# Kernel tuning notes

Measured on AMD Instinct MI355X. Metric: run time of the kernel, lower is better.

The kernel has to match this reference:

```python
import jax, jax.numpy as jnp
import numpy as np

B, IN, H, F, T = 4096, 1024, 1024, 128, 3
LN_EPS = 1e-5


def setup_inputs() -> dict:
    key = jax.random.key(0)
    ks = jax.random.split(key, 12)
    inp = {
        "input_": jax.random.normal(ks[0], (B, IN), jnp.float32),
        "hx": jax.random.normal(ks[1], (B, H), jnp.float32),
        "cx": jax.random.normal(ks[2], (B, H), jnp.float32),
        "topic_w": jax.random.uniform(ks[3], (B, T), jnp.float32),
        # factorized gate weights (init scales per reset_parameters)
        "w_ih_a": jax.random.normal(ks[4], (4 * H, F), jnp.float32) / jnp.sqrt(F),
        "w_ih_b": jnp.full((F, T), 0.1 / T, jnp.float32),
        "w_ih_c": jax.random.normal(ks[5], (F, IN), jnp.float32) / jnp.sqrt(IN),
        "w_hh_a": 0.1 * jax.random.normal(ks[6], (4 * H, F), jnp.float32),
        "w_hh_b": jnp.full((F, T), 0.1 / T, jnp.float32),
        "w_hh_c": 0.1 * jax.random.normal(ks[7], (F, H), jnp.float32),
        # theta transforms: weight=0, bias=1 per reset_parameters
        "th_ih_w": jnp.zeros((T, T), jnp.float32),
        "th_ih_b": jnp.ones((T,), jnp.float32),
        "th_hh_w": jnp.zeros((T, T), jnp.float32),
        "th_hh_b": jnp.ones((T,), jnp.float32),
        # layernorm params
        "ln_i_w": jnp.ones((4 * H,), jnp.float32),
        "ln_i_b": jnp.zeros((4 * H,), jnp.float32),
        "ln_h_w": jnp.ones((4 * H,), jnp.float32),
        "ln_h_b": jnp.zeros((4 * H,), jnp.float32),
        "ln_c_w": jnp.ones((H,), jnp.float32),
        "ln_c_b": jnp.zeros((H,), jnp.float32),
    }
    return inp


def _ln(x, w, b):
    mu = x.mean(-1, keepdims=True)
    var = ((x - mu) ** 2).mean(-1, keepdims=True)
    return (x - mu) * jax.lax.rsqrt(var + LN_EPS) * w + b


def reference(input_, hx, cx, topic_w,
              w_ih_a, w_ih_b, w_ih_c, w_hh_a, w_hh_b, w_hh_c,
              th_ih_w, th_ih_b, th_hh_w, th_hh_b,
              ln_i_w, ln_i_b, ln_h_w, ln_h_b, ln_c_w, ln_c_b):
    # factorized input gates: ((x @ C^T) * (theta(topic) @ B^T)) @ A^T
    scale_i = (topic_w @ th_ih_w.T + th_ih_b) @ w_ih_b.T            # [B, F]
    igates = ((input_ @ w_ih_c.T) * scale_i) @ w_ih_a.T             # [B, 4H]
    scale_h = (topic_w @ th_hh_w.T + th_hh_b) @ w_hh_b.T            # [B, F]
    hgates = ((hx @ w_hh_c.T) * scale_h) @ w_hh_a.T                 # [B, 4H]

    gates = _ln(igates, ln_i_w, ln_i_b) + _ln(hgates, ln_h_w, ln_h_b)
    i, f, g, o = jnp.split(gates, 4, axis=1)
    i = jax.nn.sigmoid(i)
    f = jax.nn.sigmoid(f)
    g = jnp.tanh(g)  # dropout p=0 -> identity
    o = jax.nn.sigmoid(o)
    cy = _ln(f * cx + i * g, ln_c_w, ln_c_b)
    hy = o * jnp.tanh(cy)
    return hy, cy
```

## Files before the change

### kernel.cpp

```cpp
#include <hip/hip_runtime.h>

typedef unsigned short ushort_t;
typedef __attribute__((ext_vector_type(8))) short bf8_t;
typedef __attribute__((ext_vector_type(4))) float f4_t;

#define B_   4096
#define IN_  1024
#define H_   1024
#define F_   128
#define EPS_ 1e-5f

#define NG1   512
#define NPREP 256
#define NGRAM 128

#define KC_   64
#define NCH_  16
#define XSZ_  4096
#define WSZ_  32768
#define LDSZ_ 36864

__device__ __forceinline__ float us2f(unsigned short s) {
  union { unsigned int u; float f; } v;
  v.u = ((unsigned int)s) << 16;
  return v.f;
}
__device__ __forceinline__ unsigned short f2us(float f) {
  union { float f; unsigned int u; } v;
  v.f = f;
  unsigned int r = (v.u + 0x7fffu + ((v.u >> 16) & 1u)) >> 16;
  return (unsigned short)r;
}
__device__ __forceinline__ float sigf(float x) { return 1.0f / (1.0f + __expf(-x)); }
__device__ __forceinline__ float tanh_f(float x) { return 1.0f - 2.0f / (1.0f + __expf(2.0f * x)); }

__device__ __forceinline__ int detect_fp32(const void* disc) {
  return ((const unsigned int*)disc)[0] == 0x3F800000u;
}
__device__ __forceinline__ float ldf(const void* p, int i, int fp32) {
  return fp32 ? ((const float*)p)[i] : us2f(((const ushort_t*)p)[i]);
}
__device__ __forceinline__ void ld8(const void* p, int idx, float* o, int fp32) {
  if (fp32) {
    const float4* q = (const float4*)((const float*)p + idx);
    float4 v0 = q[0], v1 = q[1];
    o[0]=v0.x; o[1]=v0.y; o[2]=v0.z; o[3]=v0.w;
    o[4]=v1.x; o[5]=v1.y; o[6]=v1.z; o[7]=v1.w;
  } else {
    uint4 v = *(const uint4*)((const ushort_t*)p + idx);
    const ushort_t* pv = (const ushort_t*)&v;
    #pragma unroll
    for (int i = 0; i < 8; i++) o[i] = us2f(pv[i]);
  }
}
__device__ __forceinline__ bf8_t cvt8p(const float* f) {
  union { bf8_t v; unsigned int u[4]; } r;
  const unsigned int* ui = (const unsigned int*)f;
  #pragma unroll
  for (int i = 0; i < 4; i++) {
    unsigned int lo = ui[2 * i] + 0x8000u;
    unsigned int hi = ui[2 * i + 1] + 0x8000u;
    r.u[i] = __builtin_amdgcn_perm(hi, lo, 0x07060302u);
  }
  return r.v;
}

__device__ __forceinline__ void gl_lds16(const void* g, void* l) {
  __builtin_amdgcn_global_load_lds(
      (const __attribute__((address_space(1))) unsigned int*)g,
      (__attribute__((address_space(3))) unsigned int*)l, 16, 0, 0);
}

__global__ __launch_bounds__(256, 4) void k_stageA(
    const void* __restrict__ X0, const void* __restrict__ X1,
    const void* __restrict__ Wc0, const void* __restrict__ Wc1,
    const void* __restrict__ Ai, const void* __restrict__ Ah,
    const void* __restrict__ lnwi, const void* __restrict__ lnwh,
    ushort_t* __restrict__ wb,
    float* __restrict__ cm_i, float* __restrict__ cm_h,
    float* __restrict__ g_i, float* __restrict__ g_h,
    float* __restrict__ C0, float* __restrict__ C1)
{
  __shared__ __align__(16) char lds_raw[LDSZ_];
  int bid = blockIdx.x, tid = threadIdx.x;
  int fp32 = detect_fp32(lnwi);

  if (bid < NG1) {
    int rb = bid >> 1, mat = bid & 1;
    const char* Xc = (const char*)(mat ? X1 : X0);
    const char* Wc = (const char*)(mat ? Wc1 : Wc0);
    float* C = mat ? C1 : C0;
    int lane = tid & 63, w = tid >> 6;
    int quad = lane >> 4, lcol = lane & 15;
    int brow0 = rb * 16;

    const char* srcp[9];
    #pragma unroll
    for (int j = 0; j < 9; j++) {
      int flat = (w * 9 + j) * 1024 + (lane << 4);
      if (flat < XSZ_) {
        int r = flat >> 8, inb = flat & 255;
        srcp[j] = Xc + (size_t)(brow0 + r) * 4096 + (inb ^ ((r & 7) << 5));
      } else {
        int fw = flat - XSZ_;
        int r = fw >> 8, inb = fw & 255;
        srcp[j] = Wc + (size_t)r * 4096 + (inb ^ ((r & 7) << 5));
      }
    }

    f4_t acc[2];
    acc[0] = (f4_t){0.f, 0.f, 0.f, 0.f};
    acc[1] = (f4_t){0.f, 0.f, 0.f, 0.f};

    for (int kc0 = 0; kc0 < NCH_; kc0++) {
      int koff = kc0 * 256;
      #pragma unroll
      for (int j = 0; j < 9; j++)
        gl_lds16(srcp[j] + koff, lds_raw + (w * 9 + j) * 1024);
      __syncthreads();

      #pragma unroll
      for (int kc = 0; kc < 2; kc++) {
        int kb = kc * 128 + quad * 32;
        int abyte = lcol * 256 + (kb ^ ((lcol & 7) << 5));
        float4 a0 = *(const float4*)(lds_raw + abyte);
        float4 a1 = *(const float4*)(lds_raw + abyte + 16);
        float a8[8] = {a0.x, a0.y, a0.z, a0.w, a1.x, a1.y, a1.z, a1.w};
        bf8_t af = cvt8p(a8);
        #pragma unroll
        for (int t = 0; t < 2; t++) {
          int f = w * 32 + t * 16 + lcol;
          int wbyte = XSZ_ + f * 256 + (kb ^ ((f & 7) << 5));
          float4 b0 = *(const float4*)(lds_raw + wbyte);
          float4 b1 = *(const float4*)(lds_raw + wbyte + 16);
          float b8[8] = {b0.x, b0.y, b0.z, b0.w, b1.x, b1.y, b1.z, b1.w};
          acc[t] = __builtin_amdgcn_mfma_f32_16x16x32_bf16(af, cvt8p(b8), acc[t], 0, 0, 0);
        }
      }
      __syncthreads();
    }

    #pragma unroll
    for (int t = 0; t < 2; t++) {
      int f = w * 32 + t * 16 + lcol;
      #pragma unroll
      for (int reg = 0; reg < 4; reg++)
        C[(brow0 + quad * 4 + reg) * F_ + f] = acc[t][reg];
    }
  } else if (bid < NG1 + NPREP) {
    int t = bid - NG1;
    #pragma unroll
    for (int i = 0; i < 16; i++) {
      int e = i * 256 + tid;
      int c = e >> 9, l = (e >> 3) & 63, j = e & 7;
      int k = c * 32 + ((l >> 4) << 3) + j;
      int n = t * 16 + (l & 15);
      float v;
      if (k < 128) v = ldf(Ai, n * F_ + k, fp32) * ldf(lnwi, n, fp32);
      else         v = ldf(Ah, n * F_ + (k - 128), fp32) * ldf(lnwh, n, fp32);
      wb[(size_t)t * 4096 + e] = f2us(v);
    }
    const void* A = (tid < 128) ? Ai : Ah;
    float* cm = (tid < 128) ? cm_i : cm_h;
    int f = tid & 127;
    float s = 0.f;
    #pragma unroll
    for (int i = 0; i < 16; i++) s += ldf(A, (t * 16 + i) * F_ + f, fp32);
    atomicAdd(&cm[f], s);
  } else {
    int g = bid - (NG1 + NPREP);
    int fblk = g & 3, mat = (g >> 2) & 1, z = g >> 3;
    const void* A = mat ? Ah : Ai;
    float* G = mat ? g_h : g_i;
    float (*As)[128] = (float(*)[128])lds_raw;
    int f1_0 = fblk * 32;
    int tf2 = tid & 31, tf1 = tid >> 5;
    float acc[4][4] = {};
    int nbase = z * 256;
    for (int n0 = nbase; n0 < nbase + 256; n0 += 32) {
      #pragma unroll
      for (int j = 0; j < 2; j++) {
        int idx = tid + 256 * j;
        int nn = idx >> 4, f8 = (idx & 15) * 8;
        float t[8];
        ld8(A, (n0 + nn) * F_ + f8, t, fp32);
        #pragma unroll
        for (int i = 0; i < 8; i++) As[nn][f8 + i] = t[i];
      }
      __syncthreads();
      #pragma unroll 4
      for (int nn = 0; nn < 32; nn++) {
        float4 a1 = *(const float4*)&As[nn][f1_0 + 4 * tf1];
        float4 a2 = *(const float4*)&As[nn][4 * tf2];
        const float* x1 = (const float*)&a1;
        const float* x2 = (const float*)&a2;
        #pragma unroll
        for (int i = 0; i < 4; i++)
          #pragma unroll
          for (int j = 0; j < 4; j++) acc[i][j] += x1[i] * x2[j];
      }
      __syncthreads();
    }
    #pragma unroll
    for (int i = 0; i < 4; i++)
      #pragma unroll
      for (int j = 0; j < 4; j++)
        atomicAdd(&G[(f1_0 + 4 * tf1 + i) * F_ + 4 * tf2 + j], acc[i][j]);
  }
}

__global__ __launch_bounds__(1024) void k_fused2(
    const float* __restrict__ C0g, const float* __restrict__ C1g,
    const float* __restrict__ g_i, const float* __restrict__ g_h,
    const float* __restrict__ cm_i, const float* __restrict__ cm_h,
    const void* __restrict__ topic,
    const void* __restrict__ thw0, const void* __restrict__ thw1,
    const void* __restrict__ thb0, const void* __restrict__ thb1,
    const void* __restrict__ wsb0, const void* __restrict__ wsb1,
    const ushort_t* __restrict__ wb,
    const void* __restrict__ lniw, const void* __restrict__ lnib,
    const void* __restrict__ lnhw, const void* __restrict__ lnhb,
    const void* __restrict__ lncw, const void* __restrict__ lncb,
    const void* __restrict__ cx, float* __restrict__ out)
{
  __shared__ float Cs[2][16][132];
  __shared__ __align__(16) ushort_t xs[4096];
  __shared__ float buf[16][1028];
  __shared__ float obuf[16][1028];
  __shared__ float p1part[2][4][16];
  __shared__ float p2s[2][16];
  __shared__ float rs2_s[2][16];
  __shared__ float mrs_s[2][16];
  __shared__ float wpart[16][16][2];
  __shared__ float mu_s[16], rs_s[16];

  int tid = threadIdx.x;
  int lane = tid & 63, w = tid >> 6;
  int quad = lane >> 4, lcol = lane & 15;
  int b0 = blockIdx.x * 16;
  int fp32 = detect_fp32(lniw);

  {
    int mat = tid >> 9, rem = tid & 511;
    int row = rem >> 5, f0 = (rem & 31) * 4;
    const float* C = mat ? C1g : C0g;
    const void* thw = mat ? thw1 : thw0;
    const void* thb = mat ? thb1 : thb0;
    const void* wbp = mat ? wsb1 : wsb0;
    float tp0 = ldf(topic, (b0 + row) * 3 + 0, fp32);
    float tp1 = ldf(topic, (b0 + row) * 3 + 1, fp32);
    float tp2 = ldf(topic, (b0 + row) * 3 + 2, fp32);
    float tv[3];
    #pragma unroll
    for (int t = 0; t < 3; t++)
      tv[t] = ldf(thb, t, fp32) + tp0 * ldf(thw, t * 3 + 0, fp32)
            + tp1 * ldf(thw, t * 3 + 1, fp32) + tp2 * ldf(thw, t * 3 + 2, fp32);
    float4 v = *(const float4*)&C[(size_t)(b0 + row) * F_ + f0];
    const float* vp = (const float*)&v;
    #pragma unroll
    for (int j = 0; j < 4; j++) {
      int f = f0 + j;
      float sc = tv[0] * ldf(wbp, f * 3 + 0, fp32)
               + tv[1] * ldf(wbp, f * 3 + 1, fp32)
               + tv[2] * ldf(wbp, f * 3 + 2, fp32);
      Cs[mat][row][f] = vp[j] * sc;
    }
  }
  __syncthreads();

  if (w < 8) {
    int w2 = w & 3, smat = w >> 2;
    const float* G  = smat ? g_h : g_i;
    const float* cm = smat ? cm_h : cm_i;
    bf8_t af[4];
    float p2p = 0.f;
    #pragma unroll
    for (int kc = 0; kc < 4; kc++) {
      int kb = kc * 32 + quad * 8;
      float a[8];
      #pragma unroll
      for (int j = 0; j < 8; j++) a[j] = Cs[smat][lcol][kb + j];
      af[kc] = cvt8p(a);
      if (w2 == 0) {
        #pragma unroll
        for (int j = 0; j < 8; j++) p2p += a[j] * cm[kb + j];
      }
    }
    float p1p[4] = {0.f, 0.f, 0.f, 0.f};
    #pragma unroll
    for (int t = 0; t < 2; t++) {
      int colf = (w2 * 2 + t) * 16 + lcol;
      f4_t acc = {0.f, 0.f, 0.f, 0.f};
      #pragma unroll
      for (int kc = 0; kc < 4; kc++) {
        const float4* qg = (const float4*)(G + colf * F_ + kc * 32 + quad * 8);
        float4 w0 = qg[0], w1 = qg[1];
        float bt[8] = {w0.x, w0.y, w0.z, w0.w, w1.x, w1.y, w1.z, w1.w};
        acc = __builtin_amdgcn_mfma_f32_16x16x32_bf16(af[kc], cvt8p(bt), acc, 0, 0, 0);
      }
      #pragma unroll
      for (int reg = 0; reg < 4; reg++)
        p1p[reg] += acc[reg] * Cs[smat][quad * 4 + reg][colf];
    }
    #pragma unroll
    for (int d = 1; d < 16; d <<= 1)
      #pragma unroll
      for (int reg = 0; reg < 4; reg++)
        p1p[reg] += __shfl_xor(p1p[reg], d, 64);
    if (lcol == 0) {
      #pragma unroll
      for (int reg = 0; reg < 4; reg++)
        p1part[smat][w2][quad * 4 + reg] = p1p[reg];
    }
    if (w2 == 0) {
      p2p += __shfl_xor(p2p, 16, 64);
      p2p += __shfl_xor(p2p, 32, 64);
      if (quad == 0) p2s[smat][lcol] = p2p;
    }
  }
  __syncthreads();
  if (tid < 32) {
    int m = tid >> 4, r = tid & 15;
    float p1 = p1part[m][0][r] + p1part[m][1][r] + p1part[m][2][r] + p1part[m][3][r];
    float E2 = p1 * (1.0f / 4096.0f);
    float mu = p2s[m][r] * (1.0f / 4096.0f);
    float rs = rsqrtf(E2 - mu * mu + EPS_);
    rs2_s[m][r] = rs;
    mrs_s[m][r] = mu * rs;
  }
  __syncthreads();

  if (tid < 512) {
    int m = tid >> 8, tt = tid & 255;
    int f = tt & 127, half = tt >> 7;
    int k = m * 128 + f;
    int c = k >> 5, lq = (k >> 3) & 3, j = k & 7;
    #pragma unroll
    for (int i = 0; i < 8; i++) {
      int r2 = half * 8 + i;
      int lfrag = r2 | (lq << 4);
      xs[c * 512 + lfrag * 8 + j] = f2us(Cs[m][r2][f] * rs2_s[m][r2]);
    }
  }
  __syncthreads();

  float mi[4], mh[4];
  #pragma unroll
  for (int reg = 0; reg < 4; reg++) {
    mi[reg] = mrs_s[0][quad * 4 + reg];
    mh[reg] = mrs_s[1][quad * 4 + reg];
  }

  float s1[4] = {0.f, 0.f, 0.f, 0.f}, s2[4] = {0.f, 0.f, 0.f, 0.f};

  #pragma unroll
  for (int q = 0; q < 4; q++) {
    int cg = w * 4 + q;
    int col = cg * 16 + lcol;
    float cxv[4];
    #pragma unroll
    for (int reg = 0; reg < 4; reg++)
      cxv[reg] = ldf(cx, (size_t)(b0 + quad * 4 + reg) * H_ + col, fp32);

    f4_t accg[4];
    #pragma unroll
    for (int g = 0; g < 4; g++) accg[g] = (f4_t){0.f, 0.f, 0.f, 0.f};
    #pragma unroll
    for (int c = 0; c < 8; c++) {
      bf8_t af = *(const bf8_t*)&xs[c * 512 + lane * 8];
      #pragma unroll
      for (int g = 0; g < 4; g++) {
        bf8_t bf = *(const bf8_t*)(wb + (size_t)(g * 64 + cg) * 4096 + c * 512 + lane * 8);
        accg[g] = __builtin_amdgcn_mfma_f32_16x16x32_bf16(af, bf, accg[g], 0, 0, 0);
      }
    }
    float liw0 = ldf(lniw, 0 * H_ + col, fp32), lib0 = ldf(lnib, 0 * H_ + col, fp32);
    float lhw0 = ldf(lnhw, 0 * H_ + col, fp32), lhb0 = ldf(lnhb, 0 * H_ + col, fp32);
    float liw1 = ldf(lniw, 1 * H_ + col, fp32), lib1 = ldf(lnib, 1 * H_ + col, fp32);
    float lhw1 = ldf(lnhw, 1 * H_ + col, fp32), lhb1 = ldf(lnhb, 1 * H_ + col, fp32);
    float liw2 = ldf(lniw, 2 * H_ + col, fp32), lib2 = ldf(lnib, 2 * H_ + col, fp32);
    float lhw2 = ldf(lnhw, 2 * H_ + col, fp32), lhb2 = ldf(lnhb, 2 * H_ + col, fp32);
    float liw3 = ldf(lniw, 3 * H_ + col, fp32), lib3 = ldf(lnib, 3 * H_ + col, fp32);
    float lhw3 = ldf(lnhw, 3 * H_ + col, fp32), lhb3 = ldf(lnhb, 3 * H_ + col, fp32);
    #pragma unroll
    for (int reg = 0; reg < 4; reg++) {
      int m = quad * 4 + reg;
      float gi = accg[0][reg] + lib0 + lhb0 - mi[reg] * liw0 - mh[reg] * lhw0;
      float gf = accg[1][reg] + lib1 + lhb1 - mi[reg] * liw1 - mh[reg] * lhw1;
      float gg = accg[2][reg] + lib2 + lhb2 - mi[reg] * liw2 - mh[reg] * lhw2;
      float go = accg[3][reg] + lib3 + lhb3 - mi[reg] * liw3 - mh[reg] * lhw3;
      float iv = sigf(gi), fv = sigf(gf), gv = tanh_f(gg), ov = sigf(go);
      float cval = fv * cxv[reg] + iv * gv;
      buf[m][col] = cval;
      obuf[m][col] = ov;
      s1[reg] += cval;
      s2[reg] += cval * cval;
    }
  }

  #pragma unroll
  for (int d = 1; d < 16; d <<= 1) {
    #pragma unroll
    for (int reg = 0; reg < 4; reg++) {
      s1[reg] += __shfl_xor(s1[reg], d, 64);
      s2[reg] += __shfl_xor(s2[reg], d, 64);
    }
  }
  if (lcol == 0) {
    #pragma unroll
    for (int reg = 0; reg < 4; reg++) {
      wpart[w][quad * 4 + reg][0] = s1[reg];
      wpart[w][quad * 4 + reg][1] = s2[reg];
    }
  }
  __syncthreads();
  if (tid < 16) {
    float t1 = 0.f, t2 = 0.f;
    #pragma unroll
    for (int ww = 0; ww < 16; ww++) { t1 += wpart[ww][tid][0]; t2 += wpart[ww][tid][1]; }
    float mu = t1 * (1.0f / 1024.0f);
    float var = t2 * (1.0f / 1024.0f) - mu * mu;
    mu_s[tid] = mu;
    rs_s[tid] = rsqrtf(var + EPS_);
  }
  __syncthreads();

  #pragma unroll
  for (int q = 0; q < 4; q++) {
    int col = (w * 4 + q) * 16 + lcol;
    float lw = ldf(lncw, col, fp32), lb = ldf(lncb, col, fp32);
    #pragma unroll
    for (int reg = 0; reg < 4; reg++) {
      int m = quad * 4 + reg;
      float cyv = (buf[m][col] - mu_s[m]) * rs_s[m] * lw + lb;
      out[(size_t)B_ * H_ + (size_t)(b0 + m) * H_ + col] = cyv;
      out[(size_t)(b0 + m) * H_ + col] = obuf[m][col] * tanh_f(cyv);
    }
  }
}

extern "C" void kernel_launch(void* const* d_in, const int* in_sizes, int n_in,
                              void* d_out, int out_size, void* d_ws, size_t ws_size,
                              hipStream_t stream) {
  const void* input_  = d_in[0];
  const void* hx      = d_in[1];
  const void* cx      = d_in[2];
  const void* topic   = d_in[3];
  const void* w_ih_a  = d_in[4];
  const void* w_ih_b  = d_in[5];
  const void* w_ih_c  = d_in[6];
  const void* w_hh_a  = d_in[7];
  const void* w_hh_b  = d_in[8];
  const void* w_hh_c  = d_in[9];
  const void* th_ih_w = d_in[10];
  const void* th_ih_b = d_in[11];
  const void* th_hh_w = d_in[12];
  const void* th_hh_b = d_in[13];
  const void* ln_i_w  = d_in[14];
  const void* ln_i_b  = d_in[15];
  const void* ln_h_w  = d_in[16];
  const void* ln_h_b  = d_in[17];
  const void* ln_c_w  = d_in[18];
  const void* ln_c_b  = d_in[19];

  float* w = (float*)d_ws;
  float* c1    = w;
  float* c2    = c1 + B_ * F_;
  float* g_i   = c2 + B_ * F_;
  float* g_h   = g_i + F_ * F_;
  float* cm_i  = g_h + F_ * F_;
  float* cm_h  = cm_i + F_;
  ushort_t* wbf = (ushort_t*)(cm_h + F_);

  hipMemsetAsync(g_i, 0, (size_t)(2 * F_ * F_ + 2 * F_) * sizeof(float), stream);

  k_stageA<<<dim3(NG1 + NPREP + NGRAM), dim3(256), 0, stream>>>(
      input_, hx, w_ih_c, w_hh_c,
      w_ih_a, w_hh_a, ln_i_w, ln_h_w,
      wbf, cm_i, cm_h, g_i, g_h, c1, c2);
  k_fused2<<<dim3(256), dim3(1024), 0, stream>>>(
      c1, c2, g_i, g_h, cm_i, cm_h,
      topic, th_ih_w, th_hh_w, th_ih_b, th_hh_b, w_ih_b, w_hh_b,
      wbf, ln_i_w, ln_i_b, ln_h_w, ln_h_b, ln_c_w, ln_c_b, cx, (float*)d_out);
}
```

Baseline: 199.7 us.

## Merge stage kernels into one cooperative kernel with grid sync

Replaces the two-kernel pipeline with a single cooperative launch of 256 blocks of 1024 threads. Within each block, waves are split by role: the first 8 do the skinny x@C^T GEMM with double-buffered direct-to-LDS loads and per-wave waits, the next 4 prepare the packed weights and column means, and the last 4 compute the Gram matrix straight from global memory. A grid sync then runs the old second-stage code. This removes one kernel launch and overlaps the prep work with the GEMM, at the cost of a grid-wide barrier, a large 1024-thread footprint and a smaller union-shared LDS region for phase one.

Result: slower. 326.0 us (+63.3%).

```diff
diff --git a/kernel.cpp b/kernel.cpp
--- a/kernel.cpp
+++ b/kernel.cpp
@@ -1,4 +1,7 @@
 #include <hip/hip_runtime.h>
+#include <hip/hip_cooperative_groups.h>
+
+namespace cg = cooperative_groups;
 
 typedef unsigned short ushort_t;
 typedef __attribute__((ext_vector_type(8))) short bf8_t;
@@ -10,16 +13,6 @@
 #define F_   128
 #define EPS_ 1e-5f
 
-#define NG1   512
-#define NPREP 256
-#define NGRAM 128
-
-#define KC_   64
-#define NCH_  16
-#define XSZ_  4096
-#define WSZ_  32768
-#define LDSZ_ 36864
-
 __device__ __forceinline__ float us2f(unsigned short s) {
   union { unsigned int u; float f; } v;
   v.u = ((unsigned int)s) << 16;
@@ -40,17 +33,13 @@
 __device__ __forceinline__ float ldf(const void* p, int i, int fp32) {
   return fp32 ? ((const float*)p)[i] : us2f(((const ushort_t*)p)[i]);
 }
-__device__ __forceinline__ void ld8(const void* p, int idx, float* o, int fp32) {
+__device__ __forceinline__ void ld4(const void* p, int idx, float* o, int fp32) {
   if (fp32) {
-    const float4* q = (const float4*)((const float*)p + idx);
-    float4 v0 = q[0], v1 = q[1];
-    o[0]=v0.x; o[1]=v0.y; o[2]=v0.z; o[3]=v0.w;
-    o[4]=v1.x; o[5]=v1.y; o[6]=v1.z; o[7]=v1.w;
+    float4 v = *(const float4*)((const float*)p + idx);
+    o[0] = v.x; o[1] = v.y; o[2] = v.z; o[3] = v.w;
   } else {
-    uint4 v = *(const uint4*)((const ushort_t*)p + idx);
-    const ushort_t* pv = (const ushort_t*)&v;
-    #pragma unroll
-    for (int i = 0; i < 8; i++) o[i] = us2f(pv[i]);
+    ushort4 v = *(const ushort4*)((const ushort_t*)p + idx);
+    o[0] = us2f(v.x); o[1] = us2f(v.y); o[2] = us2f(v.z); o[3] = us2f(v.w);
   }
 }
 __device__ __forceinline__ bf8_t cvt8p(const float* f) {
@@ -71,179 +60,159 @@
       (__attribute__((address_space(3))) unsigned int*)l, 16, 0, 0);
 }
 
-__global__ __launch_bounds__(256, 4) void k_stageA(
+union __align__(16) SharedU {
+  char p1[8][12288];
+  struct {
+    float Cs[2][16][132];
+    ushort_t xs[4096];
+    float buf[16][1028];
+    float obuf[16][1028];
+    float p1part[2][4][16];
+    float p2s[2][16];
+    float rs2[2][16];
+    float mrs[2][16];
+    float wpart[16][16][2];
+    float mu[16];
+    float rs[16];
+  } p2;
+};
+
+__global__ __launch_bounds__(1024) void k_all(
     const void* __restrict__ X0, const void* __restrict__ X1,
+    const void* __restrict__ cx, const void* __restrict__ topic,
     const void* __restrict__ Wc0, const void* __restrict__ Wc1,
     const void* __restrict__ Ai, const void* __restrict__ Ah,
-    const void* __restrict__ lnwi, const void* __restrict__ lnwh,
+    const void* __restrict__ thw0, const void* __restrict__ thw1,
+    const void* __restrict__ thb0, const void* __restrict__ thb1,
+    const void* __restrict__ wsb0, const void* __restrict__ wsb1,
+    const void* __restrict__ lniw, const void* __restrict__ lnib,
+    const void* __restrict__ lnhw, const void* __restrict__ lnhb,
+    const void* __restrict__ lncw, const void* __restrict__ lncb,
     ushort_t* __restrict__ wb,
     float* __restrict__ cm_i, float* __restrict__ cm_h,
     float* __restrict__ g_i, float* __restrict__ g_h,
-    float* __restrict__ C0, float* __restrict__ C1)
+    float* __restrict__ c1, float* __restrict__ c2,
+    float* __restrict__ out)
 {
-  __shared__ __align__(16) char lds_raw[LDSZ_];
-  int bid = blockIdx.x, tid = threadIdx.x;
-  int fp32 = detect_fp32(lnwi);
-
-  if (bid < NG1) {
-    int rb = bid >> 1, mat = bid & 1;
+  __shared__ SharedU S;
+  int tid = threadIdx.x;
+  int b = blockIdx.x;
+  int wv = tid >> 6;
+  int lane = tid & 63;
+  int quad = lane >> 4, lcol = lane & 15;
+  int fp32 = detect_fp32(lniw);
+
+  if (wv < 8) {
+    int mat = wv >> 2, ct = wv & 3;
     const char* Xc = (const char*)(mat ? X1 : X0);
     const char* Wc = (const char*)(mat ? Wc1 : Wc0);
-    float* C = mat ? C1 : C0;
-    int lane = tid & 63, w = tid >> 6;
-    int quad = lane >> 4, lcol = lane & 15;
-    int brow0 = rb * 16;
-
-    const char* srcp[9];
-    #pragma unroll
-    for (int j = 0; j < 9; j++) {
-      int flat = (w * 9 + j) * 1024 + (lane << 4);
-      if (flat < XSZ_) {
-        int r = flat >> 8, inb = flat & 255;
-        srcp[j] = Xc + (size_t)(brow0 + r) * 4096 + (inb ^ ((r & 7) << 5));
+    float* C = mat ? c2 : c1;
+    int r0 = b * 16, c0 = ct * 32;
+    char* lb = &S.p1[wv][0];
+
+    const char* sp0 = Xc + ((size_t)(r0 + lcol) * IN_ + quad * 8) * 4;
+    const char* sp2 = Wc + ((size_t)(c0 + lcol) * IN_ + quad * 8) * 4;
+    const char* sp4 = Wc + ((size_t)(c0 + 16 + lcol) * IN_ + quad * 8) * 4;
+
+    f4_t acc0 = {0.f, 0.f, 0.f, 0.f}, acc1 = {0.f, 0.f, 0.f, 0.f};
+
+#define STG_(k, half) { \
+      size_t ko_ = (size_t)(k) * 128; \
+      char* d_ = lb + (half) * 6144; \
+      gl_lds16(sp0 + ko_,      d_ + 0 * 1024 + lane * 16); \
+      gl_lds16(sp0 + ko_ + 16, d_ + 1 * 1024 + lane * 16); \
+      gl_lds16(sp2 + ko_,      d_ + 2 * 1024 + lane * 16); \
+      gl_lds16(sp2 + ko_ + 16, d_ + 3 * 1024 + lane * 16); \
+      gl_lds16(sp4 + ko_,      d_ + 4 * 1024 + lane * 16); \
+      gl_lds16(sp4 + ko_ + 16, d_ + 5 * 1024 + lane * 16); \
+    }
+    STG_(0, 0);
+    for (int k = 0; k < 32; k++) {
+      if (k + 1 < 32) {
+        STG_(k + 1, (k + 1) & 1);
+        asm volatile("s_waitcnt vmcnt(6)" ::: "memory");
       } else {
-        int fw = flat - XSZ_;
-        int r = fw >> 8, inb = fw & 255;
-        srcp[j] = Wc + (size_t)r * 4096 + (inb ^ ((r & 7) << 5));
+        asm volatile("s_waitcnt vmcnt(0)" ::: "memory");
       }
-    }
-
-    f4_t acc[2];
-    acc[0] = (f4_t){0.f, 0.f, 0.f, 0.f};
-    acc[1] = (f4_t){0.f, 0.f, 0.f, 0.f};
-
-    for (int kc0 = 0; kc0 < NCH_; kc0++) {
-      int koff = kc0 * 256;
-      #pragma unroll
-      for (int j = 0; j < 9; j++)
-        gl_lds16(srcp[j] + koff, lds_raw + (w * 9 + j) * 1024);
-      __syncthreads();
-
-      #pragma unroll
-      for (int kc = 0; kc < 2; kc++) {
-        int kb = kc * 128 + quad * 32;
-        int abyte = lcol * 256 + (kb ^ ((lcol & 7) << 5));
-        float4 a0 = *(const float4*)(lds_raw + abyte);
-        float4 a1 = *(const float4*)(lds_raw + abyte + 16);
-        float a8[8] = {a0.x, a0.y, a0.z, a0.w, a1.x, a1.y, a1.z, a1.w};
-        bf8_t af = cvt8p(a8);
-        #pragma unroll
-        for (int t = 0; t < 2; t++) {
-          int f = w * 32 + t * 16 + lcol;
-          int wbyte = XSZ_ + f * 256 + (kb ^ ((f & 7) << 5));
-          float4 b0 = *(const float4*)(lds_raw + wbyte);
-          float4 b1 = *(const float4*)(lds_raw + wbyte + 16);
-          float b8[8] = {b0.x, b0.y, b0.z, b0.w, b1.x, b1.y, b1.z, b1.w};
-          acc[t] = __builtin_amdgcn_mfma_f32_16x16x32_bf16(af, cvt8p(b8), acc[t], 0, 0, 0);
-        }
-      }
-      __syncthreads();
-    }
-
-    #pragma unroll
-    for (int t = 0; t < 2; t++) {
-      int f = w * 32 + t * 16 + lcol;
-      #pragma unroll
-      for (int reg = 0; reg < 4; reg++)
-        C[(brow0 + quad * 4 + reg) * F_ + f] = acc[t][reg];
-    }
-  } else if (bid < NG1 + NPREP) {
-    int t = bid - NG1;
+      __builtin_amdgcn_sched_barrier(0);
+      char* d = lb + (k & 1) * 6144;
+      float4 alo = *(const float4*)(d + 0 * 1024 + lane * 16);
+      float4 ahi = *(const float4*)(d + 1 * 1024 + lane * 16);
+      float a8[8] = {alo.x, alo.y, alo.z, alo.w, ahi.x, ahi.y, ahi.z, ahi.w};
+      bf8_t af = cvt8p(a8);
+      float4 b0l = *(const float4*)(d + 2 * 1024 + lane * 16);
+      float4 b0h = *(const float4*)(d + 3 * 1024 + lane * 16);
+      float b08[8] = {b0l.x, b0l.y, b0l.z, b0l.w, b0h.x, b0h.y, b0h.z, b0h.w};
+      acc0 = __builtin_amdgcn_mfma_f32_16x16x32_bf16(af, cvt8p(b08), acc0, 0, 0, 0);
+      float4 b1l = *(const float4*)(d + 4 * 1024 + lane * 16);
+      float4 b1h = *(const float4*)(d + 5 * 1024 + lane * 16);
+      float b18[8] = {b1l.x, b1l.y, b1l.z, b1l.w, b1h.x, b1h.y, b1h.z, b1h.w};
+      acc1 = __builtin_amdgcn_mfma_f32_16x16x32_bf16(af, cvt8p(b18), acc1, 0, 0, 0);
+    }
+#undef STG_
+    #pragma unroll
+    for (int reg = 0; reg < 4; reg++) {
+      int r = r0 + quad * 4 + reg;
+      C[r * F_ + c0 + lcol]      = acc0[reg];
+      C[r * F_ + c0 + 16 + lcol] = acc1[reg];
+    }
+  } else if (wv < 12) {
+    int tl = tid - 512;
     #pragma unroll
     for (int i = 0; i < 16; i++) {
-      int e = i * 256 + tid;
+      int e = i * 256 + tl;
       int c = e >> 9, l = (e >> 3) & 63, j = e & 7;
       int k = c * 32 + ((l >> 4) << 3) + j;
-      int n = t * 16 + (l & 15);
+      int n = b * 16 + (l & 15);
       float v;
-      if (k < 128) v = ldf(Ai, n * F_ + k, fp32) * ldf(lnwi, n, fp32);
-      else         v = ldf(Ah, n * F_ + (k - 128), fp32) * ldf(lnwh, n, fp32);
-      wb[(size_t)t * 4096 + e] = f2us(v);
-    }
-    const void* A = (tid < 128) ? Ai : Ah;
-    float* cm = (tid < 128) ? cm_i : cm_h;
-    int f = tid & 127;
+      if (k < 128) v = ldf(Ai, n * F_ + k, fp32) * ldf(lniw, n, fp32);
+      else         v = ldf(Ah, n * F_ + (k - 128), fp32) * ldf(lnhw, n, fp32);
+      wb[(size_t)b * 4096 + e] = f2us(v);
+    }
+    const void* A = (tl < 128) ? Ai : Ah;
+    float* cm = (tl < 128) ? cm_i : cm_h;
+    int f = tl & 127;
     float s = 0.f;
     #pragma unroll
-    for (int i = 0; i < 16; i++) s += ldf(A, (t * 16 + i) * F_ + f, fp32);
+    for (int i = 0; i < 16; i++) s += ldf(A, (b * 16 + i) * F_ + f, fp32);
     atomicAdd(&cm[f], s);
   } else {
-    int g = bid - (NG1 + NPREP);
-    int fblk = g & 3, mat = (g >> 2) & 1, z = g >> 3;
+    int u = b * 4 + (wv - 12);
+    int tile = u & 31;
+    int nsplit = u >> 5;
+    int mat = tile >> 4, f1b = (tile >> 2) & 3, f2b = tile & 3;
     const void* A = mat ? Ah : Ai;
     float* G = mat ? g_h : g_i;
-    float (*As)[128] = (float(*)[128])lds_raw;
-    int f1_0 = fblk * 32;
-    int tf2 = tid & 31, tf1 = tid >> 5;
+    int li = lane >> 3, lj = lane & 7;
+    int f1 = f1b * 32 + li * 4, f2 = f2b * 32 + lj * 4;
     float acc[4][4] = {};
-    int nbase = z * 256;
-    for (int n0 = nbase; n0 < nbase + 256; n0 += 32) {
-      #pragma unroll
-      for (int j = 0; j < 2; j++) {
-        int idx = tid + 256 * j;
-        int nn = idx >> 4, f8 = (idx & 15) * 8;
-        float t[8];
-        ld8(A, (n0 + nn) * F_ + f8, t, fp32);
+    int n0 = nsplit * 128;
+    #pragma unroll 4
+    for (int n = n0; n < n0 + 128; n++) {
+      float a1[4], a2[4];
+      ld4(A, n * F_ + f1, a1, fp32);
+      ld4(A, n * F_ + f2, a2, fp32);
+      #pragma unroll
+      for (int i = 0; i < 4; i++)
         #pragma unroll
-        for (int i = 0; i < 8; i++) As[nn][f8 + i] = t[i];
-      }
-      __syncthreads();
-      #pragma unroll 4
-      for (int nn = 0; nn < 32; nn++) {
-        float4 a1 = *(const float4*)&As[nn][f1_0 + 4 * tf1];
-        float4 a2 = *(const float4*)&As[nn][4 * tf2];
-        const float* x1 = (const float*)&a1;
-        const float* x2 = (const float*)&a2;
-        #pragma unroll
-        for (int i = 0; i < 4; i++)
-          #pragma unroll
-          for (int j = 0; j < 4; j++) acc[i][j] += x1[i] * x2[j];
-      }
-      __syncthreads();
+        for (int j = 0; j < 4; j++) acc[i][j] += a1[i] * a2[j];
     }
     #pragma unroll
     for (int i = 0; i < 4; i++)
       #pragma unroll
       for (int j = 0; j < 4; j++)
-        atomicAdd(&G[(f1_0 + 4 * tf1 + i) * F_ + 4 * tf2 + j], acc[i][j]);
-  }
-}
-
-__global__ __launch_bounds__(1024) void k_fused2(
-    const float* __restrict__ C0g, const float* __restrict__ C1g,
-    const float* __restrict__ g_i, const float* __restrict__ g_h,
-    const float* __restrict__ cm_i, const float* __restrict__ cm_h,
-    const void* __restrict__ topic,
-    const void* __restrict__ thw0, const void* __restrict__ thw1,
-    const void* __restrict__ thb0, const void* __restrict__ thb1,
-    const void* __restrict__ wsb0, const void* __restrict__ wsb1,
-    const ushort_t* __restrict__ wb,
-    const void* __restrict__ lniw, const void* __restrict__ lnib,
-    const void* __restrict__ lnhw, const void* __restrict__ lnhb,
-    const void* __restrict__ lncw, const void* __restrict__ lncb,
-    const void* __restrict__ cx, float* __restrict__ out)
-{
-  __shared__ float Cs[2][16][132];
-  __shared__ __align__(16) ushort_t xs[4096];
-  __shared__ float buf[16][1028];
-  __shared__ float obuf[16][1028];
-  __shared__ float p1part[2][4][16];
-  __shared__ float p2s[2][16];
-  __shared__ float rs2_s[2][16];
-  __shared__ float mrs_s[2][16];
-  __shared__ float wpart[16][16][2];
-  __shared__ float mu_s[16], rs_s[16];
-
-  int tid = threadIdx.x;
-  int lane = tid & 63, w = tid >> 6;
-  int quad = lane >> 4, lcol = lane & 15;
-  int b0 = blockIdx.x * 16;
-  int fp32 = detect_fp32(lniw);
+        atomicAdd(&G[(f1 + i) * F_ + f2 + j], acc[i][j]);
+  }
+
+  cg::this_grid().sync();
+
+  int w = wv;
+  int b0 = b * 16;
 
   {
     int mat = tid >> 9, rem = tid & 511;
     int row = rem >> 5, f0 = (rem & 31) * 4;
-    const float* C = mat ? C1g : C0g;
+    const float* C = mat ? c2 : c1;
     const void* thw = mat ? thw1 : thw0;
     const void* thb = mat ? thb1 : thb0;
     const void* wbp = mat ? wsb1 : wsb0;
@@ -263,7 +232,7 @@
       float sc = tv[0] * ldf(wbp, f * 3 + 0, fp32)
                + tv[1] * ldf(wbp, f * 3 + 1, fp32)
                + tv[2] * ldf(wbp, f * 3 + 2, fp32);
-      Cs[mat][row][f] = vp[j] * sc;
+      S.p2.Cs[mat][row][f] = vp[j] * sc;
     }
   }
   __syncthreads();
@@ -279,7 +248,7 @@
       int kb = kc * 32 + quad * 8;
       float a[8];
       #pragma unroll
-      for (int j = 0; j < 8; j++) a[j] = Cs[smat][lcol][kb + j];
+      for (int j = 0; j < 8; j++) a[j] = S.p2.Cs[smat][lcol][kb + j];
       af[kc] = cvt8p(a);
       if (w2 == 0) {
         #pragma unroll
@@ -300,7 +269,7 @@
       }
       #pragma unroll
       for (int reg = 0; reg < 4; reg++)
-        p1p[reg] += acc[reg] * Cs[smat][quad * 4 + reg][colf];
+        p1p[reg] += acc[reg] * S.p2.Cs[smat][quad * 4 + reg][colf];
     }
     #pragma unroll
     for (int d = 1; d < 16; d <<= 1)
@@ -310,23 +279,24 @@
     if (lcol == 0) {
       #pragma unroll
       for (int reg = 0; reg < 4; reg++)
-        p1part[smat][w2][quad * 4 + reg] = p1p[reg];
+        S.p2.p1part[smat][w2][quad * 4 + reg] = p1p[reg];
     }
     if (w2 == 0) {
       p2p += __shfl_xor(p2p, 16, 64);
       p2p += __shfl_xor(p2p, 32, 64);
-      if (quad == 0) p2s[smat][lcol] = p2p;
+      if (quad == 0) S.p2.p2s[smat][lcol] = p2p;
     }
   }
   __syncthreads();
   if (tid < 32) {
     int m = tid >> 4, r = tid & 15;
-    float p1 = p1part[m][0][r] + p1part[m][1][r] + p1part[m][2][r] + p1part[m][3][r];
+    float p1 = S.p2.p1part[m][0][r] + S.p2.p1part[m][1][r]
+             + S.p2.p1part[m][2][r] + S.p2.p1part[m][3][r];
     float E2 = p1 * (1.0f / 4096.0f);
-    float mu = p2s[m][r] * (1.0f / 4096.0f);
-    float rs = rsqrtf(E2 - mu * mu + EPS_);
-    rs2_s[m][r] = rs;
-    mrs_s[m][r] = mu * rs;
+    float mu = S.p2.p2s[m][r] * (1.0f / 4096.0f);
+    float rsv = rsqrtf(E2 - mu * mu + EPS_);
+    S.p2.rs2[m][r] = rsv;
+    S.p2.mrs[m][r] = mu * rsv;
   }
   __syncthreads();
 
@@ -339,7 +309,7 @@
     for (int i = 0; i < 8; i++) {
       int r2 = half * 8 + i;
       int lfrag = r2 | (lq << 4);
-      xs[c * 512 + lfrag * 8 + j] = f2us(Cs[m][r2][f] * rs2_s[m][r2]);
+      S.p2.xs[c * 512 + lfrag * 8 + j] = f2us(S.p2.Cs[m][r2][f] * S.p2.rs2[m][r2]);
     }
   }
   __syncthreads();
@@ -347,16 +317,16 @@
   float mi[4], mh[4];
   #pragma unroll
   for (int reg = 0; reg < 4; reg++) {
-    mi[reg] = mrs_s[0][quad * 4 + reg];
-    mh[reg] = mrs_s[1][quad * 4 + reg];
+    mi[reg] = S.p2.mrs[0][quad * 4 + reg];
+    mh[reg] = S.p2.mrs[1][quad * 4 + reg];
   }
 
   float s1[4] = {0.f, 0.f, 0.f, 0.f}, s2[4] = {0.f, 0.f, 0.f, 0.f};
 
   #pragma unroll
   for (int q = 0; q < 4; q++) {
-    int cg = w * 4 + q;
-    int col = cg * 16 + lcol;
+    int cg2 = w * 4 + q;
+    int col = cg2 * 16 + lcol;
     float cxv[4];
     #pragma unroll
     for (int reg = 0; reg < 4; reg++)
@@ -367,10 +337,10 @@
     for (int g = 0; g < 4; g++) accg[g] = (f4_t){0.f, 0.f, 0.f, 0.f};
     #pragma unroll
     for (int c = 0; c < 8; c++) {
-      bf8_t af = *(const bf8_t*)&xs[c * 512 + lane * 8];
+      bf8_t af = *(const bf8_t*)&S.p2.xs[c * 512 + lane * 8];
       #pragma unroll
       for (int g = 0; g < 4; g++) {
-        bf8_t bf = *(const bf8_t*)(wb + (size_t)(g * 64 + cg) * 4096 + c * 512 + lane * 8);
+        bf8_t bf = *(const bf8_t*)(wb + (size_t)(g * 64 + cg2) * 4096 + c * 512 + lane * 8);
         accg[g] = __builtin_amdgcn_mfma_f32_16x16x32_bf16(af, bf, accg[g], 0, 0, 0);
       }
     }
@@ -391,8 +361,8 @@
       float go = accg[3][reg] + lib3 + lhb3 - mi[reg] * liw3 - mh[reg] * lhw3;
       float iv = sigf(gi), fv = sigf(gf), gv = tanh_f(gg), ov = sigf(go);
       float cval = fv * cxv[reg] + iv * gv;
-      buf[m][col] = cval;
-      obuf[m][col] = ov;
+      S.p2.buf[m][col] = cval;
+      S.p2.obuf[m][col] = ov;
       s1[reg] += cval;
       s2[reg] += cval * cval;
     }
@@ -409,19 +379,22 @@
   if (lcol == 0) {
     #pragma unroll
     for (int reg = 0; reg < 4; reg++) {
-      wpart[w][quad * 4 + reg][0] = s1[reg];
-      wpart[w][quad * 4 + reg][1] = s2[reg];
+      S.p2.wpart[w][quad * 4 + reg][0] = s1[reg];
+      S.p2.wpart[w][quad * 4 + reg][1] = s2[reg];
     }
   }
   __syncthreads();
   if (tid < 16) {
     float t1 = 0.f, t2 = 0.f;
     #pragma unroll
-    for (int ww = 0; ww < 16; ww++) { t1 += wpart[ww][tid][0]; t2 += wpart[ww][tid][1]; }
+    for (int ww = 0; ww < 16; ww++) {
+      t1 += S.p2.wpart[ww][tid][0];
+      t2 += S.p2.wpart[ww][tid][1];
+    }
     float mu = t1 * (1.0f / 1024.0f);
     float var = t2 * (1.0f / 1024.0f) - mu * mu;
-    mu_s[tid] = mu;
-    rs_s[tid] = rsqrtf(var + EPS_);
+    S.p2.mu[tid] = mu;
+    S.p2.rs[tid] = rsqrtf(var + EPS_);
   }
   __syncthreads();
 
@@ -432,9 +405,9 @@
     #pragma unroll
     for (int reg = 0; reg < 4; reg++) {
       int m = quad * 4 + reg;
-      float cyv = (buf[m][col] - mu_s[m]) * rs_s[m] * lw + lb;
+      float cyv = (S.p2.buf[m][col] - S.p2.mu[m]) * S.p2.rs[m] * lw + lb;
       out[(size_t)B_ * H_ + (size_t)(b0 + m) * H_ + col] = cyv;
-      out[(size_t)(b0 + m) * H_ + col] = obuf[m][col] * tanh_f(cyv);
+      out[(size_t)(b0 + m) * H_ + col] = S.p2.obuf[m][col] * tanh_f(cyv);
     }
   }
 }
@@ -471,15 +444,20 @@
   float* cm_i  = g_h + F_ * F_;
   float* cm_h  = cm_i + F_;
   ushort_t* wbf = (ushort_t*)(cm_h + F_);
+  float* outp = (float*)d_out;
 
   hipMemsetAsync(g_i, 0, (size_t)(2 * F_ * F_ + 2 * F_) * sizeof(float), stream);
 
-  k_stageA<<<dim3(NG1 + NPREP + NGRAM), dim3(256), 0, stream>>>(
-      input_, hx, w_ih_c, w_hh_c,
-      w_ih_a, w_hh_a, ln_i_w, ln_h_w,
-      wbf, cm_i, cm_h, g_i, g_h, c1, c2);
-  k_fused2<<<dim3(256), dim3(1024), 0, stream>>>(
-      c1, c2, g_i, g_h, cm_i, cm_h,
-      topic, th_ih_w, th_hh_w, th_ih_b, th_hh_b, w_ih_b, w_hh_b,
-      wbf, ln_i_w, ln_i_b, ln_h_w, ln_h_b, ln_c_w, ln_c_b, cx, (float*)d_out);
-}
+  void* args[] = {
+    (void*)&input_, (void*)&hx, (void*)&cx, (void*)&topic,
+    (void*)&w_ih_c, (void*)&w_hh_c, (void*)&w_ih_a, (void*)&w_hh_a,
+    (void*)&th_ih_w, (void*)&th_hh_w, (void*)&th_ih_b, (void*)&th_hh_b,
+    (void*)&w_ih_b, (void*)&w_hh_b,
+    (void*)&ln_i_w, (void*)&ln_i_b, (void*)&ln_h_w, (void*)&ln_h_b,
+    (void*)&ln_c_w, (void*)&ln_c_b,
+    (void*)&wbf, (void*)&cm_i, (void*)&cm_h,
+    (void*)&g_i, (void*)&g_h, (void*)&c1, (void*)&c2, (void*)&outp };
+
+  hipLaunchCooperativeKernel((const void*)k_all, dim3(256), dim3(1024),
+                             args, 0, stream);
+}
```
